# Performance work log

Hardware: AMD Instinct MI355X
Metric: run time of the kernel (lower is better)

## Reference

```python
import jax, jax.numpy as jnp
import numpy as np


def setup_inputs() -> dict:
    key = jax.random.key(0)
    ks = jax.random.split(key, 10)
    N, OUT, IN = 8, 4096, 4096
    B, S = 8, 2048
    return {
        "x": jax.random.normal(ks[0], (B, S, IN), dtype=jnp.float32),
        "weight": jax.random.normal(ks[1], (OUT, IN), dtype=jnp.float32) * 0.02,
        "bias": jax.random.normal(ks[2], (OUT,), dtype=jnp.float32) * 0.02,
        "scale": jax.random.normal(ks[3], (N,), dtype=jnp.float32) * 0.01,
        "wq": jax.random.randint(ks[4], (N, OUT, IN), 0, 256, dtype=jnp.int32),
        "wscale": jax.random.uniform(ks[5], (N,), dtype=jnp.float32) * 0.001,
        "wzp": jax.random.randint(ks[6], (N,), 0, 256, dtype=jnp.int32),
        "bq": jax.random.randint(ks[7], (N, OUT), 0, 256, dtype=jnp.int32),
        "bscale": jax.random.uniform(ks[8], (N,), dtype=jnp.float32) * 0.001,
        "bzp": jax.random.randint(ks[9], (N,), 0, 256, dtype=jnp.int32),
    }


def reference(x, weight, bias, scale, wq, wscale, wzp, bq, bscale, bzp):
    # Dequant: pert_i = wq_i * wscale_i + wzp_i  (per slot i)
    # Weighted sum over slots: sum_i scale_i * pert_i
    #   = einsum('i,ijk->jk', scale*wscale, wq) + (scale . wzp) broadcast
    f32 = jnp.float32
    dW = jnp.einsum('i,ijk->jk', scale * wscale, wq.astype(f32)) \
         + jnp.dot(scale, wzp.astype(f32))  # scalar zero-point term
    W = weight + dW
    db = jnp.einsum('i,ij->j', scale * bscale, bq.astype(f32)) \
         + jnp.dot(scale, bzp.astype(f32))
    b = bias + db
    # F.linear: x @ W^T + b
    return jnp.einsum('bsi,oi->bso', x, W) + b
```

## Files before the change

### kernel.cpp

```cpp
#include <hip/hip_runtime.h>
#include <stdint.h>
#include <stddef.h>

#define NSLOT 8
#define OUTF  4096
#define INF   4096
#define MDIM  16384
#define KDIM  4096
#define NDIM  4096
#define NTILE (KDIM / 64)

typedef __bf16 bf16x8 __attribute__((ext_vector_type(8)));
typedef float f32x4 __attribute__((ext_vector_type(4)));
typedef unsigned short u16x8 __attribute__((ext_vector_type(8)));

__device__ __forceinline__ unsigned short f2bf(float f) {
  unsigned u = __builtin_bit_cast(unsigned, f);
  u += 0x7fffu + ((u >> 16) & 1u);
  return (unsigned short)(u >> 16);
}

__global__ void coeff_kernel(const float* __restrict__ scale,
                             const float* __restrict__ wscale,
                             const int* __restrict__ wzp,
                             const float* __restrict__ bscale,
                             const int* __restrict__ bzp,
                             float* __restrict__ co) {
  if (threadIdx.x == 0) {
    float c = 0.f, cb = 0.f;
    for (int i = 0; i < NSLOT; ++i) {
      co[i]     = scale[i] * wscale[i];
      co[9 + i] = scale[i] * bscale[i];
      c  += scale[i] * (float)wzp[i];
      cb += scale[i] * (float)bzp[i];
    }
    co[8]  = c;
    co[17] = cb;
  }
}

__global__ __launch_bounds__(256) void dequant_w(const float* __restrict__ weight,
                                                 const int* __restrict__ wq,
                                                 const float* __restrict__ co,
                                                 unsigned short* __restrict__ wd) {
  const size_t base = ((size_t)blockIdx.x * 256 + threadIdx.x) * 8;
  const float c = co[8];
  float4 w0 = *(const float4*)(weight + base);
  float4 w1 = *(const float4*)(weight + base + 4);
  float acc[8] = {w0.x + c, w0.y + c, w0.z + c, w0.w + c,
                  w1.x + c, w1.y + c, w1.z + c, w1.w + c};
#pragma unroll
  for (int i = 0; i < NSLOT; ++i) {
    const float a = co[i];
    const int* q = wq + (size_t)i * ((size_t)OUTF * INF) + base;
    int4 q0 = *(const int4*)q;
    int4 q1 = *(const int4*)(q + 4);
    acc[0] += a * (float)q0.x; acc[1] += a * (float)q0.y;
    acc[2] += a * (float)q0.z; acc[3] += a * (float)q0.w;
    acc[4] += a * (float)q1.x; acc[5] += a * (float)q1.y;
    acc[6] += a * (float)q1.z; acc[7] += a * (float)q1.w;
  }
  u16x8 p;
#pragma unroll
  for (int e = 0; e < 8; ++e) p[e] = f2bf(acc[e]);
  *(u16x8*)(wd + base) = p;
}

__global__ __launch_bounds__(256) void xconv(const float* __restrict__ x,
                                             unsigned short* __restrict__ xb) {
  const size_t base = ((size_t)blockIdx.x * 256 + threadIdx.x) * 8;
  float4 v0 = *(const float4*)(x + base);
  float4 v1 = *(const float4*)(x + base + 4);
  u16x8 p;
  p[0] = f2bf(v0.x); p[1] = f2bf(v0.y); p[2] = f2bf(v0.z); p[3] = f2bf(v0.w);
  p[4] = f2bf(v1.x); p[5] = f2bf(v1.y); p[6] = f2bf(v1.z); p[7] = f2bf(v1.w);
  *(u16x8*)(xb + base) = p;
}

__global__ __launch_bounds__(256) void bias_fuse(const float* __restrict__ bias,
                                                 const int* __restrict__ bq,
                                                 const float* __restrict__ co,
                                                 float* __restrict__ bv) {
  const int o = blockIdx.x * 256 + threadIdx.x;
  float acc = bias[o] + co[17];
#pragma unroll
  for (int i = 0; i < NSLOT; ++i)
    acc += co[9 + i] * (float)bq[i * OUTF + o];
  bv[o] = acc;
}

__global__ __launch_bounds__(512, 2) void gemm256(const unsigned short* __restrict__ A,
                                                  const unsigned short* __restrict__ Bw,
                                                  const float* __restrict__ bv,
                                                  float* __restrict__ C) {
  __shared__ __attribute__((aligned(16))) unsigned short sA[2 * 16384];
  __shared__ __attribute__((aligned(16))) unsigned short sB[2 * 16384];

  const int tid  = threadIdx.x;
  const int lane = tid & 63;
  const int wave = tid >> 6;
  const int wm   = (wave >> 2) * 128;
  const int wn   = (wave & 3) * 64;

  const int bid = blockIdx.x;
  const int wg  = ((bid & 7) << 7) | (bid >> 3);
  const int m0  = (wg >> 4) << 8;
  const int n0  = (wg & 15) << 8;

  const int fr   = lane & 15;
  const int q    = lane >> 4;
  const int fx8  = (fr & 7) << 3;
  const int qa0  = (q << 3) ^ fx8;
  const int qa1  = ((4 + q) << 3) ^ fx8;
  const int rowA = (wm + fr) << 6;
  const int rowB = (wn + fr) << 6;

  const int srow = tid >> 3;
  const int scol = ((tid & 7) ^ (srow & 7)) << 3;
  const unsigned short* gA = A  + (size_t)(m0 + srow) * KDIM + scol;
  const unsigned short* gB = Bw + (size_t)(n0 + srow) * KDIM + scol;

  f32x4 acc[8][4] = {};

#define STAGE_A(kt, b)                                                          \
  {                                                                             \
    _Pragma("unroll")                                                           \
    for (int j = 0; j < 4; ++j)                                                 \
      __builtin_amdgcn_global_load_lds(                                         \
          (const __attribute__((address_space(1))) void*)(gA + (size_t)(kt) * 64 + (size_t)j * 64 * KDIM), \
          (__attribute__((address_space(3))) void*)(sA + (b) * 16384 + j * 4096 + tid * 8), 16, 0, 0); \
  }
#define STAGE_B(kt, b)                                                          \
  {                                                                             \
    _Pragma("unroll")                                                           \
    for (int j = 0; j < 4; ++j)                                                 \
      __builtin_amdgcn_global_load_lds(                                         \
          (const __attribute__((address_space(1))) void*)(gB + (size_t)(kt) * 64 + (size_t)j * 64 * KDIM), \
          (__attribute__((address_space(3))) void*)(sB + (b) * 16384 + j * 4096 + tid * 8), 16, 0, 0); \
  }

#define MFMA4(ii, AF, BF)                                                       \
  {                                                                             \
    _Pragma("unroll")                                                           \
    for (int j = 0; j < 4; ++j)                                                 \
      acc[ii][j] = __builtin_amdgcn_mfma_f32_16x16x32_bf16(AF, BF[j], acc[ii][j], 0, 0, 0); \
  }

  STAGE_A(0, 0);
  STAGE_B(0, 0);
  asm volatile("s_waitcnt vmcnt(0)" ::: "memory");
  __builtin_amdgcn_sched_barrier(0);
  __builtin_amdgcn_s_barrier();

  for (int t = 0; t < NTILE; ++t) {
    const int cur = t & 1;
    const unsigned short* bufA = sA + cur * 16384;
    const unsigned short* bufB = sB + cur * 16384;
    bf16x8 bf0[4], bf1[4];

    {
      bf16x8 x00 = *(const bf16x8*)(bufA + rowA + 0 * 1024 + qa0);
      bf16x8 x01 = *(const bf16x8*)(bufA + rowA + 0 * 1024 + qa1);
      bf16x8 x10 = *(const bf16x8*)(bufA + rowA + 1 * 1024 + qa0);
      bf16x8 x11 = *(const bf16x8*)(bufA + rowA + 1 * 1024 + qa1);
#pragma unroll
      for (int j = 0; j < 4; ++j) {
        bf0[j] = *(const bf16x8*)(bufB + rowB + j * 1024 + qa0);
        bf1[j] = *(const bf16x8*)(bufB + rowB + j * 1024 + qa1);
      }
      if (t + 1 < NTILE) STAGE_A(t + 1, cur ^ 1);
      __builtin_amdgcn_s_barrier();
      __builtin_amdgcn_sched_barrier(0);
      __builtin_amdgcn_s_setprio(1);
      MFMA4(0, x00, bf0); MFMA4(1, x10, bf0);
      MFMA4(0, x01, bf1); MFMA4(1, x11, bf1);
      __builtin_amdgcn_s_setprio(0);
      __builtin_amdgcn_s_barrier();
    }
    {
      bf16x8 x00 = *(const bf16x8*)(bufA + rowA + 2 * 1024 + qa0);
      bf16x8 x01 = *(const bf16x8*)(bufA + rowA + 2 * 1024 + qa1);
      bf16x8 x10 = *(const bf16x8*)(bufA + rowA + 3 * 1024 + qa0);
      bf16x8 x11 = *(const bf16x8*)(bufA + rowA + 3 * 1024 + qa1);
      if (t + 1 < NTILE) STAGE_B(t + 1, cur ^ 1);
      __builtin_amdgcn_s_barrier();
      __builtin_amdgcn_sched_barrier(0);
      __builtin_amdgcn_s_setprio(1);
      MFMA4(2, x00, bf0); MFMA4(3, x10, bf0);
      MFMA4(2, x01, bf1); MFMA4(3, x11, bf1);
      __builtin_amdgcn_s_setprio(0);
      __builtin_amdgcn_s_barrier();
    }
    {
      bf16x8 x00 = *(const bf16x8*)(bufA + rowA + 4 * 1024 + qa0);
      bf16x8 x01 = *(const bf16x8*)(bufA + rowA + 4 * 1024 + qa1);
      bf16x8 x10 = *(const bf16x8*)(bufA + rowA + 5 * 1024 + qa0);
      bf16x8 x11 = *(const bf16x8*)(bufA + rowA + 5 * 1024 + qa1);
      __builtin_amdgcn_s_barrier();
      __builtin_amdgcn_sched_barrier(0);
      __builtin_amdgcn_s_setprio(1);
      MFMA4(4, x00, bf0); MFMA4(5, x10, bf0);
      MFMA4(4, x01, bf1); MFMA4(5, x11, bf1);
      __builtin_amdgcn_s_setprio(0);
      __builtin_amdgcn_s_barrier();
    }
    {
      bf16x8 x00 = *(const bf16x8*)(bufA + rowA + 6 * 1024 + qa0);
      bf16x8 x01 = *(const bf16x8*)(bufA + rowA + 6 * 1024 + qa1);
      bf16x8 x10 = *(const bf16x8*)(bufA + rowA + 7 * 1024 + qa0);
      bf16x8 x11 = *(const bf16x8*)(bufA + rowA + 7 * 1024 + qa1);
      __builtin_amdgcn_s_barrier();
      __builtin_amdgcn_sched_barrier(0);
      __builtin_amdgcn_s_setprio(1);
      MFMA4(6, x00, bf0); MFMA4(7, x10, bf0);
      MFMA4(6, x01, bf1); MFMA4(7, x11, bf1);
      __builtin_amdgcn_s_setprio(0);
      asm volatile("s_waitcnt vmcnt(0)" ::: "memory");
      __builtin_amdgcn_sched_barrier(0);
      __builtin_amdgcn_s_barrier();
    }
  }

  const int r0 = m0 + wm + ((lane >> 4) << 2);
  const int c0 = n0 + wn + (lane & 15);
#pragma unroll
  for (int j = 0; j < 4; ++j) {
    const int col = c0 + j * 16;
    const float bb = bv[col];
#pragma unroll
    for (int i = 0; i < 8; ++i) {
      const int row = r0 + i * 16;
#pragma unroll
      for (int r = 0; r < 4; ++r)
        C[(size_t)(row + r) * NDIM + col] = acc[i][j][r] + bb;
    }
  }
#undef STAGE_A
#undef STAGE_B
#undef MFMA4
}

extern "C" void kernel_launch(void* const* d_in, const int* in_sizes, int n_in,
                              void* d_out, int out_size, void* d_ws, size_t ws_size,
                              hipStream_t stream) {
  const float* x      = (const float*)d_in[0];
  const float* weight = (const float*)d_in[1];
  const float* bias   = (const float*)d_in[2];
  const float* scale  = (const float*)d_in[3];
  const int*   wq     = (const int*)d_in[4];
  const float* wscale = (const float*)d_in[5];
  const int*   wzp    = (const int*)d_in[6];
  const int*   bq     = (const int*)d_in[7];
  const float* bscale = (const float*)d_in[8];
  const int*   bzp    = (const int*)d_in[9];
  float* out = (float*)d_out;

  char* ws = (char*)d_ws;
  unsigned short* wd = (unsigned short*)(ws);
  unsigned short* xb = (unsigned short*)(ws + 33554432);
  float* bv = (float*)(ws + 33554432 + 134217728);
  float* co = (float*)(ws + 33554432 + 134217728 + 16384);

  coeff_kernel<<<1, 64, 0, stream>>>(scale, wscale, wzp, bscale, bzp, co);
  dequant_w<<<(OUTF * (size_t)INF) / 8 / 256, 256, 0, stream>>>(weight, wq, co, wd);
  xconv<<<((size_t)MDIM * KDIM) / 8 / 256, 256, 0, stream>>>(x, xb);
  bias_fuse<<<OUTF / 256, 256, 0, stream>>>(bias, bq, co, bv);
  gemm256<<<dim3((MDIM / 256) * (NDIM / 256)), 512, 0, stream>>>(xb, wd, bv, out);
}
```

Baseline: 1.575 ms.

## Software-pipeline LDS A-fragment reads across MFMA phases and merge prep kernels

The GEMM main loop now prefetches the next A-fragment pair from LDS while the current MFMA phase runs, double-buffering A registers. It also preloads the first pair of the next tile before the loop back-edge, which cuts the barriers per k-tile from eight to four. Separately, the weight dequant, x conversion and bias kernels are merged into one launch to save launch gaps. The trade-off is more register pressure from the extra live A fragments, and the reordered barriers could expose LDS hazards.

```diff
diff --git a/kernel.cpp b/kernel.cpp
--- a/kernel.cpp
+++ b/kernel.cpp
@@ -39,54 +39,54 @@
   }
 }
 
-__global__ __launch_bounds__(256) void dequant_w(const float* __restrict__ weight,
-                                                 const int* __restrict__ wq,
-                                                 const float* __restrict__ co,
-                                                 unsigned short* __restrict__ wd) {
-  const size_t base = ((size_t)blockIdx.x * 256 + threadIdx.x) * 8;
-  const float c = co[8];
-  float4 w0 = *(const float4*)(weight + base);
-  float4 w1 = *(const float4*)(weight + base + 4);
-  float acc[8] = {w0.x + c, w0.y + c, w0.z + c, w0.w + c,
-                  w1.x + c, w1.y + c, w1.z + c, w1.w + c};
-#pragma unroll
-  for (int i = 0; i < NSLOT; ++i) {
-    const float a = co[i];
-    const int* q = wq + (size_t)i * ((size_t)OUTF * INF) + base;
-    int4 q0 = *(const int4*)q;
-    int4 q1 = *(const int4*)(q + 4);
-    acc[0] += a * (float)q0.x; acc[1] += a * (float)q0.y;
-    acc[2] += a * (float)q0.z; acc[3] += a * (float)q0.w;
-    acc[4] += a * (float)q1.x; acc[5] += a * (float)q1.y;
-    acc[6] += a * (float)q1.z; acc[7] += a * (float)q1.w;
-  }
-  u16x8 p;
-#pragma unroll
-  for (int e = 0; e < 8; ++e) p[e] = f2bf(acc[e]);
-  *(u16x8*)(wd + base) = p;
-}
-
-__global__ __launch_bounds__(256) void xconv(const float* __restrict__ x,
-                                             unsigned short* __restrict__ xb) {
-  const size_t base = ((size_t)blockIdx.x * 256 + threadIdx.x) * 8;
-  float4 v0 = *(const float4*)(x + base);
-  float4 v1 = *(const float4*)(x + base + 4);
-  u16x8 p;
-  p[0] = f2bf(v0.x); p[1] = f2bf(v0.y); p[2] = f2bf(v0.z); p[3] = f2bf(v0.w);
-  p[4] = f2bf(v1.x); p[5] = f2bf(v1.y); p[6] = f2bf(v1.z); p[7] = f2bf(v1.w);
-  *(u16x8*)(xb + base) = p;
-}
-
-__global__ __launch_bounds__(256) void bias_fuse(const float* __restrict__ bias,
-                                                 const int* __restrict__ bq,
-                                                 const float* __restrict__ co,
-                                                 float* __restrict__ bv) {
-  const int o = blockIdx.x * 256 + threadIdx.x;
-  float acc = bias[o] + co[17];
-#pragma unroll
-  for (int i = 0; i < NSLOT; ++i)
-    acc += co[9 + i] * (float)bq[i * OUTF + o];
-  bv[o] = acc;
+__global__ __launch_bounds__(256) void prep(const float* __restrict__ weight,
+                                            const int* __restrict__ wq,
+                                            const float* __restrict__ co,
+                                            unsigned short* __restrict__ wd,
+                                            const float* __restrict__ x,
+                                            unsigned short* __restrict__ xb,
+                                            const float* __restrict__ bias,
+                                            const int* __restrict__ bq,
+                                            float* __restrict__ bv) {
+  const int b = blockIdx.x;
+  if (b < 8192) {
+    const size_t base = ((size_t)b * 256 + threadIdx.x) * 8;
+    const float c = co[8];
+    float4 w0 = *(const float4*)(weight + base);
+    float4 w1 = *(const float4*)(weight + base + 4);
+    float acc[8] = {w0.x + c, w0.y + c, w0.z + c, w0.w + c,
+                    w1.x + c, w1.y + c, w1.z + c, w1.w + c};
+#pragma unroll
+    for (int i = 0; i < NSLOT; ++i) {
+      const float a = co[i];
+      const int* q = wq + (size_t)i * ((size_t)OUTF * INF) + base;
+      int4 q0 = *(const int4*)q;
+      int4 q1 = *(const int4*)(q + 4);
+      acc[0] += a * (float)q0.x; acc[1] += a * (float)q0.y;
+      acc[2] += a * (float)q0.z; acc[3] += a * (float)q0.w;
+      acc[4] += a * (float)q1.x; acc[5] += a * (float)q1.y;
+      acc[6] += a * (float)q1.z; acc[7] += a * (float)q1.w;
+    }
+    u16x8 p;
+#pragma unroll
+    for (int e = 0; e < 8; ++e) p[e] = f2bf(acc[e]);
+    *(u16x8*)(wd + base) = p;
+  } else if (b < 8192 + 32768) {
+    const size_t base = ((size_t)(b - 8192) * 256 + threadIdx.x) * 8;
+    float4 v0 = *(const float4*)(x + base);
+    float4 v1 = *(const float4*)(x + base + 4);
+    u16x8 p;
+    p[0] = f2bf(v0.x); p[1] = f2bf(v0.y); p[2] = f2bf(v0.z); p[3] = f2bf(v0.w);
+    p[4] = f2bf(v1.x); p[5] = f2bf(v1.y); p[6] = f2bf(v1.z); p[7] = f2bf(v1.w);
+    *(u16x8*)(xb + base) = p;
+  } else {
+    const int o = (b - 40960) * 256 + threadIdx.x;
+    float acc = bias[o] + co[17];
+#pragma unroll
+    for (int i = 0; i < NSLOT; ++i)
+      acc += co[9 + i] * (float)bq[i * OUTF + o];
+    bv[o] = acc;
+  }
 }
 
 __global__ __launch_bounds__(512, 2) void gemm256(const unsigned short* __restrict__ A,
@@ -139,86 +139,77 @@
           (__attribute__((address_space(3))) void*)(sB + (b) * 16384 + j * 4096 + tid * 8), 16, 0, 0); \
   }
 
-#define MFMA4(ii, AF, BF)                                                       \
+#define MFMA_PHASE(r0, r1, A0, A1, A2, A3)                                      \
   {                                                                             \
     _Pragma("unroll")                                                           \
     for (int j = 0; j < 4; ++j)                                                 \
-      acc[ii][j] = __builtin_amdgcn_mfma_f32_16x16x32_bf16(AF, BF[j], acc[ii][j], 0, 0, 0); \
-  }
+      acc[r0][j] = __builtin_amdgcn_mfma_f32_16x16x32_bf16(A0, bf0[j], acc[r0][j], 0, 0, 0); \
+    _Pragma("unroll")                                                           \
+    for (int j = 0; j < 4; ++j)                                                 \
+      acc[r1][j] = __builtin_amdgcn_mfma_f32_16x16x32_bf16(A2, bf0[j], acc[r1][j], 0, 0, 0); \
+    _Pragma("unroll")                                                           \
+    for (int j = 0; j < 4; ++j)                                                 \
+      acc[r0][j] = __builtin_amdgcn_mfma_f32_16x16x32_bf16(A1, bf1[j], acc[r0][j], 0, 0, 0); \
+    _Pragma("unroll")                                                           \
+    for (int j = 0; j < 4; ++j)                                                 \
+      acc[r1][j] = __builtin_amdgcn_mfma_f32_16x16x32_bf16(A3, bf1[j], acc[r1][j], 0, 0, 0); \
+  }
+
+#define READ_APAIR(d0, d1, d2, d3, buf, p)                                      \
+  d0 = *(const bf16x8*)((buf) + rowA + (2 * (p)) * 1024 + qa0);                 \
+  d1 = *(const bf16x8*)((buf) + rowA + (2 * (p)) * 1024 + qa1);                 \
+  d2 = *(const bf16x8*)((buf) + rowA + (2 * (p) + 1) * 1024 + qa0);             \
+  d3 = *(const bf16x8*)((buf) + rowA + (2 * (p) + 1) * 1024 + qa1);
 
   STAGE_A(0, 0);
   STAGE_B(0, 0);
   asm volatile("s_waitcnt vmcnt(0)" ::: "memory");
-  __builtin_amdgcn_sched_barrier(0);
   __builtin_amdgcn_s_barrier();
+
+  bf16x8 aP0, aP1, aP2, aP3, aQ0, aQ1, aQ2, aQ3;
+  bf16x8 bf0[4], bf1[4];
+  READ_APAIR(aP0, aP1, aP2, aP3, sA, 0);
 
   for (int t = 0; t < NTILE; ++t) {
     const int cur = t & 1;
-    const unsigned short* bufA = sA + cur * 16384;
-    const unsigned short* bufB = sB + cur * 16384;
-    bf16x8 bf0[4], bf1[4];
-
-    {
-      bf16x8 x00 = *(const bf16x8*)(bufA + rowA + 0 * 1024 + qa0);
-      bf16x8 x01 = *(const bf16x8*)(bufA + rowA + 0 * 1024 + qa1);
-      bf16x8 x10 = *(const bf16x8*)(bufA + rowA + 1 * 1024 + qa0);
-      bf16x8 x11 = *(const bf16x8*)(bufA + rowA + 1 * 1024 + qa1);
-#pragma unroll
-      for (int j = 0; j < 4; ++j) {
-        bf0[j] = *(const bf16x8*)(bufB + rowB + j * 1024 + qa0);
-        bf1[j] = *(const bf16x8*)(bufB + rowB + j * 1024 + qa1);
-      }
-      if (t + 1 < NTILE) STAGE_A(t + 1, cur ^ 1);
-      __builtin_amdgcn_s_barrier();
-      __builtin_amdgcn_sched_barrier(0);
-      __builtin_amdgcn_s_setprio(1);
-      MFMA4(0, x00, bf0); MFMA4(1, x10, bf0);
-      MFMA4(0, x01, bf1); MFMA4(1, x11, bf1);
-      __builtin_amdgcn_s_setprio(0);
-      __builtin_amdgcn_s_barrier();
-    }
-    {
-      bf16x8 x00 = *(const bf16x8*)(bufA + rowA + 2 * 1024 + qa0);
-      bf16x8 x01 = *(const bf16x8*)(bufA + rowA + 2 * 1024 + qa1);
-      bf16x8 x10 = *(const bf16x8*)(bufA + rowA + 3 * 1024 + qa0);
-      bf16x8 x11 = *(const bf16x8*)(bufA + rowA + 3 * 1024 + qa1);
-      if (t + 1 < NTILE) STAGE_B(t + 1, cur ^ 1);
-      __builtin_amdgcn_s_barrier();
-      __builtin_amdgcn_sched_barrier(0);
-      __builtin_amdgcn_s_setprio(1);
-      MFMA4(2, x00, bf0); MFMA4(3, x10, bf0);
-      MFMA4(2, x01, bf1); MFMA4(3, x11, bf1);
-      __builtin_amdgcn_s_setprio(0);
-      __builtin_amdgcn_s_barrier();
-    }
-    {
-      bf16x8 x00 = *(const bf16x8*)(bufA + rowA + 4 * 1024 + qa0);
-      bf16x8 x01 = *(const bf16x8*)(bufA + rowA + 4 * 1024 + qa1);
-      bf16x8 x10 = *(const bf16x8*)(bufA + rowA + 5 * 1024 + qa0);
-      bf16x8 x11 = *(const bf16x8*)(bufA + rowA + 5 * 1024 + qa1);
-      __builtin_amdgcn_s_barrier();
-      __builtin_amdgcn_sched_barrier(0);
-      __builtin_amdgcn_s_setprio(1);
-      MFMA4(4, x00, bf0); MFMA4(5, x10, bf0);
-      MFMA4(4, x01, bf1); MFMA4(5, x11, bf1);
-      __builtin_amdgcn_s_setprio(0);
-      __builtin_amdgcn_s_barrier();
-    }
-    {
-      bf16x8 x00 = *(const bf16x8*)(bufA + rowA + 6 * 1024 + qa0);
-      bf16x8 x01 = *(const bf16x8*)(bufA + rowA + 6 * 1024 + qa1);
-      bf16x8 x10 = *(const bf16x8*)(bufA + rowA + 7 * 1024 + qa0);
-      bf16x8 x11 = *(const bf16x8*)(bufA + rowA + 7 * 1024 + qa1);
-      __builtin_amdgcn_s_barrier();
-      __builtin_amdgcn_sched_barrier(0);
-      __builtin_amdgcn_s_setprio(1);
-      MFMA4(6, x00, bf0); MFMA4(7, x10, bf0);
-      MFMA4(6, x01, bf1); MFMA4(7, x11, bf1);
-      __builtin_amdgcn_s_setprio(0);
-      asm volatile("s_waitcnt vmcnt(0)" ::: "memory");
-      __builtin_amdgcn_sched_barrier(0);
-      __builtin_amdgcn_s_barrier();
-    }
+    const int nb  = cur ^ 1;
+    const unsigned short* bufA  = sA + cur * 16384;
+    const unsigned short* bufB  = sB + cur * 16384;
+    const unsigned short* nbufA = sA + nb * 16384;
+    const bool pf = (t + 1 < NTILE);
+
+    if (pf) STAGE_A(t + 1, nb);
+#pragma unroll
+    for (int j = 0; j < 4; ++j) {
+      bf0[j] = *(const bf16x8*)(bufB + rowB + j * 1024 + qa0);
+      bf1[j] = *(const bf16x8*)(bufB + rowB + j * 1024 + qa1);
+    }
+    __builtin_amdgcn_s_setprio(1);
+    MFMA_PHASE(0, 1, aP0, aP1, aP2, aP3);
+    __builtin_amdgcn_s_setprio(0);
+    READ_APAIR(aQ0, aQ1, aQ2, aQ3, bufA, 1);
+    __builtin_amdgcn_s_barrier();
+
+    if (pf) STAGE_B(t + 1, nb);
+    __builtin_amdgcn_s_setprio(1);
+    MFMA_PHASE(2, 3, aQ0, aQ1, aQ2, aQ3);
+    __builtin_amdgcn_s_setprio(0);
+    READ_APAIR(aP0, aP1, aP2, aP3, bufA, 2);
+    __builtin_amdgcn_s_barrier();
+
+    __builtin_amdgcn_s_setprio(1);
+    MFMA_PHASE(4, 5, aP0, aP1, aP2, aP3);
+    __builtin_amdgcn_s_setprio(0);
+    READ_APAIR(aQ0, aQ1, aQ2, aQ3, bufA, 3);
+    asm volatile("s_waitcnt vmcnt(0)" ::: "memory");
+    __builtin_amdgcn_s_barrier();
+    __builtin_amdgcn_sched_barrier(0);
+
+    __builtin_amdgcn_s_setprio(1);
+    MFMA_PHASE(6, 7, aQ0, aQ1, aQ2, aQ3);
+    __builtin_amdgcn_s_setprio(0);
+    if (pf) { READ_APAIR(aP0, aP1, aP2, aP3, nbufA, 0); }
+    __builtin_amdgcn_s_barrier();
   }
 
   const int r0 = m0 + wm + ((lane >> 4) << 2);
@@ -237,7 +228,8 @@
   }
 #undef STAGE_A
 #undef STAGE_B
-#undef MFMA4
+#undef MFMA_PHASE
+#undef READ_APAIR
 }
 
 extern "C" void kernel_launch(void* const* d_in, const int* in_sizes, int n_in,
@@ -262,8 +254,6 @@
   float* co = (float*)(ws + 33554432 + 134217728 + 16384);
 
   coeff_kernel<<<1, 64, 0, stream>>>(scale, wscale, wzp, bscale, bzp, co);
-  dequant_w<<<(OUTF * (size_t)INF) / 8 / 256, 256, 0, stream>>>(weight, wq, co, wd);
-  xconv<<<((size_t)MDIM * KDIM) / 8 / 256, 256, 0, stream>>>(x, xb);
-  bias_fuse<<<OUTF / 256, 256, 0, stream>>>(bias, bq, co, bv);
+  prep<<<8192 + 32768 + 16, 256, 0, stream>>>(weight, wq, co, wd, x, xb, bias, bq, bv);
   gemm256<<<dim3((MDIM / 256) * (NDIM / 256)), 512, 0, stream>>>(xb, wd, bv, out);
 }
```

Result: no change. 1.556 ms (-1.2%).
